# Optimization experiments

Measured on AMD Instinct MI355X. Metric: run time of the kernel, lower is better.

The kernel has to match this reference:

```python
import jax, jax.numpy as jnp
import numpy as np

# ---- static config ----
B, N, C, HF, WF = 2, 256, 256, 64, 64
PATCH = 512
ROI = 15
MARGIN = (ROI - 1) // 2
HID = 256
HEADS = 8
DEPTH = 3
FFN = 1024
NQ = 16
LN_EPS = 1e-5


def setup_inputs() -> dict:
    key = jax.random.key(0)
    ks = jax.random.split(key, 16)
    p = lambda i, shape: (0.02 * jax.random.normal(ks[i], shape, jnp.float32))
    inp = {
        "image_embeddings": jax.random.normal(ks[0], (B, C, HF, WF), jnp.float32),
        "keypoints": jax.random.uniform(ks[1], (B, N, 2), jnp.float32, 0.0, float(PATCH)),
        "keypoints_valid_mask": jax.random.randint(ks[2], (B, N), 0, 2) == 1,
        "proj_w": p(3, (HID, C)), "proj_b": jnp.zeros((HID,), jnp.float32),
        "query_embed": p(4, (NQ, HID)),
        "self_qkv_w": p(5, (DEPTH, 3 * HID, HID)), "self_qkv_b": jnp.zeros((DEPTH, 3 * HID), jnp.float32),
        "self_out_w": p(6, (DEPTH, HID, HID)), "self_out_b": jnp.zeros((DEPTH, HID), jnp.float32),
        "cross_qkv_w": p(7, (DEPTH, 3 * HID, HID)), "cross_qkv_b": jnp.zeros((DEPTH, 3 * HID), jnp.float32),
        "cross_out_w": p(8, (DEPTH, HID, HID)), "cross_out_b": jnp.zeros((DEPTH, HID), jnp.float32),
        "ffn1_w": p(9, (DEPTH, FFN, HID)), "ffn1_b": jnp.zeros((DEPTH, FFN), jnp.float32),
        "ffn2_w": p(10, (DEPTH, HID, FFN)), "ffn2_b": jnp.zeros((DEPTH, HID), jnp.float32),
        "ln1_w": jnp.ones((DEPTH, HID), jnp.float32), "ln1_b": jnp.zeros((DEPTH, HID), jnp.float32),
        "ln2_w": jnp.ones((DEPTH, HID), jnp.float32), "ln2_b": jnp.zeros((DEPTH, HID), jnp.float32),
        "ln3_w": jnp.ones((DEPTH, HID), jnp.float32), "ln3_b": jnp.zeros((DEPTH, HID), jnp.float32),
        "out_w": p(11, (4, HID)), "out_b": jnp.zeros((4,), jnp.float32),
    }
    return inp


def _layer_norm(x, w, b):
    mu = x.mean(-1, keepdims=True)
    var = ((x - mu) ** 2).mean(-1, keepdims=True)
    return (x - mu) * jax.lax.rsqrt(var + LN_EPS) * w + b


def _mha(q_in, kv_in, Wqkv, bqkv, Wo, bo, pad=None):
    # PyTorch nn.MultiheadAttention math (batch_first). pad: [B, S_kv] True=masked.
    Dh = HID // HEADS
    Wq, Wk, Wv = jnp.split(Wqkv, 3, axis=0)
    bq, bk, bv = jnp.split(bqkv, 3, axis=0)
    Bsz = q_in.shape[0]
    q = (q_in @ Wq.T + bq).reshape(Bsz, -1, HEADS, Dh)
    k = (kv_in @ Wk.T + bk).reshape(Bsz, -1, HEADS, Dh)
    v = (kv_in @ Wv.T + bv).reshape(Bsz, -1, HEADS, Dh)
    s = jnp.einsum('bqhd,bkhd->bhqk', q, k) * (Dh ** -0.5)
    if pad is not None:
        s = jnp.where(pad[:, None, None, :], -jnp.inf, s)
    a = jax.nn.softmax(s, axis=-1)
    o = jnp.einsum('bhqk,bkhd->bqhd', a, v).reshape(Bsz, -1, HID)
    return o @ Wo.T + bo


def _roi_sample(img, keypoints):
    # _get_valid_grid + F.grid_sample(bilinear, align_corners=False, zeros padding)
    rc = jnp.round(keypoints)                               # [B,N,2] (r,c), round-half-even like Python round
    off = jnp.arange(-MARGIN, MARGIN + 1, dtype=img.dtype)  # [ROI]
    gy = rc[:, :, 0][..., None, None] + off[:, None]        # [B,N,ROI,ROI] rows
    gx = rc[:, :, 1][..., None, None] + off[None, :]        # [B,N,ROI,ROI] cols
    gxn = gx / (PATCH - 1) * 2.0 - 1.0
    gyn = gy / (PATCH - 1) * 2.0 - 1.0
    invalid = (gxn < -1) | (gyn < -1) | (gxn > 1) | (gyn > 1)  # [B,N,ROI,ROI]
    gxn = jnp.where(invalid, 0.0, gxn)
    gyn = jnp.where(invalid, 0.0, gyn)
    # unnormalize onto the feature map (align_corners=False)
    x = ((gxn + 1.0) * WF - 1.0) * 0.5
    y = ((gyn + 1.0) * HF - 1.0) * 0.5
    x = x.reshape(B, -1)  # [B, P], P = N*ROI*ROI
    y = y.reshape(B, -1)
    x0f = jnp.floor(x); y0f = jnp.floor(y)
    wx = x - x0f; wy = y - y0f
    x0 = x0f.astype(jnp.int32); y0 = y0f.astype(jnp.int32)
    bidx = jnp.arange(B)[:, None]

    def tap(yi, xi, w):
        ok = (yi >= 0) & (yi < HF) & (xi >= 0) & (xi < WF)
        yc = jnp.clip(yi, 0, HF - 1)
        xc = jnp.clip(xi, 0, WF - 1)
        v = img[bidx, :, yc, xc]                 # [B,P,C] gather
        return v * (w * ok)[..., None]

    out = (tap(y0, x0, (1 - wy) * (1 - wx)) + tap(y0, x0 + 1, (1 - wy) * wx)
           + tap(y0 + 1, x0, wy * (1 - wx)) + tap(y0 + 1, x0 + 1, wy * wx))
    feat = out.reshape(B, N, ROI * ROI, C)
    feat = jnp.where(invalid.reshape(B, N, ROI * ROI)[..., None], 0.0, feat)
    return feat  # [B, N, HW, C]


def reference(image_embeddings, keypoints, keypoints_valid_mask, proj_w, proj_b,
              query_embed, self_qkv_w, self_qkv_b, self_out_w, self_out_b,
              cross_qkv_w, cross_qkv_b, cross_out_w, cross_out_b,
              ffn1_w, ffn1_b, ffn2_w, ffn2_b,
              ln1_w, ln1_b, ln2_w, ln2_b, ln3_w, ln3_b, out_w, out_b):
    feat = _roi_sample(image_embeddings, keypoints)                 # [B,N,HW,C]
    mem = jnp.einsum('bnpc,oc->bnpo', feat, proj_w) + proj_b        # 1x1 conv proj
    mem = mem.reshape(B * N, ROI * ROI, HID)
    pad = jnp.broadcast_to(~keypoints_valid_mask.reshape(-1, 1), (B * N, ROI * ROI))
    pad = pad.at[:, 0].set(False)                                    # token 0 always attendable
    tgt = jnp.broadcast_to(query_embed[None], (B * N, NQ, HID))
    for l in range(DEPTH):  # post-norm TransformerDecoderLayer, relu, eval (no dropout)
        sa = _mha(tgt, tgt, self_qkv_w[l], self_qkv_b[l], self_out_w[l], self_out_b[l])
        tgt = _layer_norm(tgt + sa, ln1_w[l], ln1_b[l])
        ca = _mha(tgt, mem, cross_qkv_w[l], cross_qkv_b[l], cross_out_w[l], cross_out_b[l], pad)
        tgt = _layer_norm(tgt + ca, ln2_w[l], ln2_b[l])
        ff = jax.nn.relu(tgt @ ffn1_w[l].T + ffn1_b[l]) @ ffn2_w[l].T + ffn2_b[l]
        tgt = _layer_norm(tgt + ff, ln3_w[l], ln3_b[l])
    out = tgt @ out_w.T + out_b                                      # [B*N, NQ, 4]
    return out.reshape(B, N, NQ, 4)
```

## Files before the change

### kernel.cpp

```cpp
#include <hip/hip_runtime.h>
#include <hip/hip_fp16.h>

#define LB __launch_bounds__(256)

typedef unsigned short u16;
typedef unsigned int   u32;
typedef __attribute__((ext_vector_type(8))) short bf16x8;
typedef __attribute__((ext_vector_type(4))) float f32x4;
typedef __attribute__((ext_vector_type(8))) u16  u16x8;

__device__ __forceinline__ u16 f2b(float f) {
    u32 u = __float_as_uint(f);
    u32 r = (u + 0x7fffu + ((u >> 16) & 1u)) >> 16;
    return (u16)r;
}
__device__ __forceinline__ float b2f(u16 h) {
    return __uint_as_float((u32)h << 16);
}

#define QSCALE 0.17677669529663687f


__global__ LB void k_wconv(const float* __restrict__ s0, const float* __restrict__ s1,
                           const float* __restrict__ s2, const float* __restrict__ s3,
                           const float* __restrict__ s4, const float* __restrict__ s5,
                           const float* __restrict__ s6, u16* __restrict__ dst,
                           const unsigned char* __restrict__ m, int* __restrict__ valid,
                           const float* __restrict__ pb,
                           const float* __restrict__ cqkv_b,
                           float* __restrict__ ckv)
{
    if (blockIdx.x >= 14336) {
        const int pblk = blockIdx.x - 14336;
        if (pblk == 0) {
            __shared__ int flag;
            if (threadIdx.x == 0) flag = 0;
            __syncthreads();
            int loc = 0;
            for (int off = threadIdx.x; off < 512; off += 256)
                if ((off & 3) != 0 && m[off] != 0) loc = 1;
            if (loc) atomicOr(&flag, 1);
            __syncthreads();
            const bool bytelay = (flag != 0);
            for (int s = threadIdx.x; s < 512; s += 256)
                valid[s] = bytelay ? (int)(m[s] != 0) : (int)(((const int*)m)[s] != 0);
        } else {
            const int l = pblk - 1;
            const float* Wv = s3 + (size_t)l * 196608 + 131072;
            const float* vb = cqkv_b + (size_t)l * 768 + 512;
            const int o = threadIdx.x;
            float c = 0.f;
            for (int cc = 0; cc < 256; cc += 4) {
                const float4 p4 = *(const float4*)(pb + cc);
                const float4 v4 = *(const float4*)(Wv + (size_t)o * 256 + cc);
                c += p4.x * v4.x + p4.y * v4.y + p4.z * v4.z + p4.w * v4.w;
            }
            ckv[l * 512 + o]       = cqkv_b[(size_t)l * 768 + o];
            ckv[l * 512 + 256 + o] = c + vb[o];
        }
        return;
    }
    const int e = blockIdx.x * 256 + threadIdx.x;
    if (e >= 3670016) return;
    float v;
    int i = e;
    if (i < 65536) v = s0[i];
    else if ((i -= 65536) < 589824) v = s1[i];
    else if ((i -= 589824) < 196608) v = s2[i];
    else if ((i -= 196608) < 589824) v = s3[i];
    else if ((i -= 589824) < 196608) v = s4[i];
    else if ((i -= 196608) < 786432) v = s5[i];
    else if ((i -= 786432) < 786432) v = s6[i];
    else if ((i -= 786432) < 393216) {
        const int l = i / 131072;
        const int r = (i - l * 131072) >> 8;
        const int c = i & 255;
        v = s3[(size_t)l * 196608 + (size_t)(256 + r) * 256 + c];
    } else {
        i -= 393216;
        v = s0[(i & 255) * 256 + (i >> 8)];
    }
    dst[e] = f2b(v);
}

__global__ LB void k_transpose(const float* __restrict__ img, u16* __restrict__ imgTb)
{
    __shared__ float tile[64][65];
    const int b  = blockIdx.z;
    const int c0 = blockIdx.y * 64;
    const int p0 = blockIdx.x * 64;
    const int t  = threadIdx.x;
    const int tr = t >> 6, tc = t & 63;
#pragma unroll
    for (int p = 0; p < 16; ++p) {
        const int i = p * 4 + tr;
        tile[i][tc] = img[((size_t)(b * 256 + c0 + i)) * 4096 + p0 + tc];
    }
    __syncthreads();
#pragma unroll
    for (int p = 0; p < 16; ++p) {
        const int jj = p * 4 + tr;
        imgTb[((size_t)(b * 4096 + p0 + jj)) * 256 + c0 + tc] = f2b(tile[tc][jj]);
    }
}

template<int BM>
__global__ LB void gemm_mfma(const u16* __restrict__ A, const u16* __restrict__ W,
                             const float* __restrict__ bias,
                             float* __restrict__ Cf, u16* __restrict__ Cb,
                             int M, int N, int K, int relu)
{
    constexpr int BN = 128;
    __shared__ u16 lds[2][(BM + BN) * 64];
    const int t = threadIdx.x;
    const int wid = t >> 6, lane = t & 63;
    const int bm = blockIdx.y * BM, bn = blockIdx.x * BN;
    const int KT = K >> 6;

    auto stage = [&](int buf, int kt) {
        const int k0 = kt * 64;
        const int rr = t >> 3;
        const int u  = t & 7;
#pragma unroll
        for (int q = 0; q < BM / 32; ++q) {
            const int r = q * 32 + rr;
            const u16* src = A + (size_t)(bm + r) * K + k0 + ((u ^ (r & 7)) << 3);
            __builtin_amdgcn_global_load_lds(
                (const __attribute__((address_space(1))) void*)src,
                (__attribute__((address_space(3))) void*)&lds[buf][q * 2048 + wid * 512],
                16, 0, 0);
        }
#pragma unroll
        for (int q = 0; q < 4; ++q) {
            const int r = q * 32 + rr;
            const u16* src = W + (size_t)(bn + r) * K + k0 + ((u ^ (r & 7)) << 3);
            __builtin_amdgcn_global_load_lds(
                (const __attribute__((address_space(1))) void*)src,
                (__attribute__((address_space(3))) void*)&lds[buf][BM * 64 + q * 2048 + wid * 512],
                16, 0, 0);
        }
    };

    const int wr = wid >> 1, wc = wid & 1;
    constexpr int MR = BM / 32;
    f32x4 acc[MR][4];
    const f32x4 z = {0.f, 0.f, 0.f, 0.f};
#pragma unroll
    for (int mi = 0; mi < MR; ++mi)
#pragma unroll
        for (int ni = 0; ni < 4; ++ni) acc[mi][ni] = z;

    const int r16 = lane & 15, kg = lane >> 4;

    stage(0, 0);
    int cur = 0;
    for (int kt = 0; kt < KT; ++kt) {
        asm volatile("s_waitcnt vmcnt(0)" ::: "memory");
        __syncthreads();
        if (kt + 1 < KT) stage(cur ^ 1, kt + 1);
        const u16* pA = lds[cur];
        const u16* pB = lds[cur] + BM * 64;
#pragma unroll
        for (int kk = 0; kk < 2; ++kk) {
            const int s = kk * 4 + kg;
            bf16x8 afr[MR], bfr[4];
#pragma unroll
            for (int mi = 0; mi < MR; ++mi) {
                const int r = wr * (BM / 2) + mi * 16 + r16;
                afr[mi] = *(const bf16x8*)(pA + r * 64 + ((s ^ (r & 7)) << 3));
            }
#pragma unroll
            for (int ni = 0; ni < 4; ++ni) {
                const int c = wc * 64 + ni * 16 + r16;
                bfr[ni] = *(const bf16x8*)(pB + c * 64 + ((s ^ (c & 7)) << 3));
            }
#pragma unroll
            for (int mi = 0; mi < MR; ++mi)
#pragma unroll
                for (int ni = 0; ni < 4; ++ni)
                    acc[mi][ni] = __builtin_amdgcn_mfma_f32_16x16x32_bf16(
                        afr[mi], bfr[ni], acc[mi][ni], 0, 0, 0);
        }
        cur ^= 1;
    }

#pragma unroll
    for (int mi = 0; mi < MR; ++mi) {
#pragma unroll
        for (int ni = 0; ni < 4; ++ni) {
            const int col = bn + wc * 64 + ni * 16 + r16;
            const float bs = bias ? bias[col] : 0.0f;
#pragma unroll
            for (int rg = 0; rg < 4; ++rg) {
                const int row = bm + wr * (BM / 2) + mi * 16 + kg * 4 + rg;
                float v = acc[mi][ni][rg] + bs;
                if (relu) v = fmaxf(v, 0.0f);
                if (Cf) Cf[(size_t)row * N + col] = v;
                if (Cb) Cb[(size_t)row * N + col] = f2b(v);
            }
        }
    }
}

__global__ LB void gemm_ln(const u16* __restrict__ A, const u16* __restrict__ W,
                           const float* __restrict__ bias,
                           float* __restrict__ tgt, u16* __restrict__ tgtb,
                           const float* __restrict__ lnw, const float* __restrict__ lnb,
                           int K,
                           const float* __restrict__ ow, const float* __restrict__ ob,
                           float* __restrict__ outp)
{
    __shared__ u16 lA[32 * 64];
    __shared__ u16 lB[256 * 64];
    __shared__ float psum[2][32];
    __shared__ float psq[2][32];
    __shared__ float hsum[2][32][4];
    const int t = threadIdx.x;
    const int wid = t >> 6, lane = t & 63;
    const int r16 = lane & 15, kg = lane >> 4;
    const int wr = wid >> 1, wc = wid & 1;
    const int bm = blockIdx.x * 32;
    const int KT = K >> 6;

    f32x4 acc[8];
    const f32x4 z = {0.f, 0.f, 0.f, 0.f};
#pragma unroll
    for (int ni = 0; ni < 8; ++ni) acc[ni] = z;

    for (int kt = 0; kt < KT; ++kt) {
        const int k0 = kt * 64;
        const int rr = t >> 3;
        const int u  = t & 7;
        {
            const int r = rr;
            const u16* src = A + (size_t)(bm + r) * K + k0 + ((u ^ (r & 7)) << 3);
            __builtin_amdgcn_global_load_lds(
                (const __attribute__((address_space(1))) void*)src,
                (__attribute__((address_space(3))) void*)&lA[wid * 512],
                16, 0, 0);
        }
#pragma unroll
        for (int q = 0; q < 8; ++q) {
            const int r = q * 32 + rr;
            const u16* src = W + (size_t)r * K + k0 + ((u ^ (r & 7)) << 3);
            __builtin_amdgcn_global_load_lds(
                (const __attribute__((address_space(1))) void*)src,
                (__attribute__((address_space(3))) void*)&lB[q * 2048 + wid * 512],
                16, 0, 0);
        }
        asm volatile("s_waitcnt vmcnt(0)" ::: "memory");
        __syncthreads();
#pragma unroll
        for (int kk = 0; kk < 2; ++kk) {
            const int s = kk * 4 + kg;
            const int ra = wr * 16 + r16;
            const bf16x8 afr = *(const bf16x8*)(lA + ra * 64 + ((s ^ (ra & 7)) << 3));
#pragma unroll
            for (int ni = 0; ni < 8; ++ni) {
                const int c = wc * 128 + ni * 16 + r16;
                const bf16x8 bfr = *(const bf16x8*)(lB + c * 64 + ((s ^ (c & 7)) << 3));
                acc[ni] = __builtin_amdgcn_mfma_f32_16x16x32_bf16(afr, bfr, acc[ni], 0, 0, 0);
            }
        }
        __syncthreads();
    }

    float xv[4][8];
    float bcol[8], wcol[8], bncol[8];
#pragma unroll
    for (int ni = 0; ni < 8; ++ni) {
        const int c = wc * 128 + ni * 16 + r16;
        bcol[ni]  = bias[c];
        wcol[ni]  = lnw[c];
        bncol[ni] = lnb[c];
    }
#pragma unroll
    for (int rg = 0; rg < 4; ++rg) {
        const int row = bm + wr * 16 + kg * 4 + rg;
#pragma unroll
        for (int ni = 0; ni < 8; ++ni) {
            const int c = wc * 128 + ni * 16 + r16;
            xv[rg][ni] = tgt[(size_t)row * 256 + c] + acc[ni][rg] + bcol[ni];
        }
    }
#pragma unroll
    for (int rg = 0; rg < 4; ++rg) {
        float s = 0.f;
#pragma unroll
        for (int ni = 0; ni < 8; ++ni) s += xv[rg][ni];
#pragma unroll
        for (int m = 1; m < 16; m <<= 1) s += __shfl_xor(s, m);
        if (r16 == 0) psum[wc][wr * 16 + kg * 4 + rg] = s;
    }
    __syncthreads();
    float mu[4];
#pragma unroll
    for (int rg = 0; rg < 4; ++rg) {
        const int rl = wr * 16 + kg * 4 + rg;
        mu[rg] = (psum[0][rl] + psum[1][rl]) * (1.0f / 256.0f);
    }
#pragma unroll
    for (int rg = 0; rg < 4; ++rg) {
        float q = 0.f;
#pragma unroll
        for (int ni = 0; ni < 8; ++ni) {
            const float d = xv[rg][ni] - mu[rg];
            q += d * d;
        }
#pragma unroll
        for (int m = 1; m < 16; m <<= 1) q += __shfl_xor(q, m);
        if (r16 == 0) psq[wc][wr * 16 + kg * 4 + rg] = q;
    }
    __syncthreads();
    float onorm[4][8];
#pragma unroll
    for (int rg = 0; rg < 4; ++rg) {
        const int rl = wr * 16 + kg * 4 + rg;
        const int row = bm + rl;
        const float var = (psq[0][rl] + psq[1][rl]) * (1.0f / 256.0f);
        const float inv = 1.0f / sqrtf(var + 1e-5f);
#pragma unroll
        for (int ni = 0; ni < 8; ++ni) {
            const int c = wc * 128 + ni * 16 + r16;
            const float o = (xv[rg][ni] - mu[rg]) * inv * wcol[ni] + bncol[ni];
            onorm[rg][ni] = o;
            tgt[(size_t)row * 256 + c]  = o;
            tgtb[(size_t)row * 256 + c] = f2b(o);
        }
    }

    if (outp) {
#pragma unroll
        for (int j = 0; j < 4; ++j) {
            float wj[8];
#pragma unroll
            for (int ni = 0; ni < 8; ++ni)
                wj[ni] = ow[j * 256 + wc * 128 + ni * 16 + r16];
#pragma unroll
            for (int rg = 0; rg < 4; ++rg) {
                float p = 0.f;
#pragma unroll
                for (int ni = 0; ni < 8; ++ni) p += onorm[rg][ni] * wj[ni];
#pragma unroll
                for (int m = 1; m < 16; m <<= 1) p += __shfl_xor(p, m);
                if (r16 == 0) hsum[wc][wr * 16 + kg * 4 + rg][j] = p;
            }
        }
        __syncthreads();
        if (t < 128) {
            const int row = t >> 2, j = t & 3;
            outp[(size_t)(bm + row) * 4 + j] =
                hsum[0][row][j] + hsum[1][row][j] + ob[j];
        }
    }
}

__global__ LB void k_init_tgt(float* __restrict__ tgt, u16* __restrict__ tgtb,
                              const float* __restrict__ qe)
{
    const int e = blockIdx.x * 256 + threadIdx.x;
    const int c = e & 255;
    const int row = e >> 8;
    const int i = row & 15;
    const float v = qe[(i << 8) | c];
    tgt[e] = v;
    tgtb[e] = f2b(v);
}

__global__ LB void k_self_attn(const u16* __restrict__ QKV, u16* __restrict__ O)
{
    __shared__ __align__(16) u16 arena[4][1536];
    const int t = threadIdx.x;
    const int lane = t & 63, wid = t >> 6;
    const int r16 = lane & 15, kg = lane >> 4;
    const int blk = blockIdx.x;
    const int s = blk >> 1;
    const int h = (blk & 1) * 4 + wid;

    u16* p_lds = &arena[wid][0];
    u16* vT    = &arena[wid][512];

    const bf16x8 qfr = *(const bf16x8*)(QKV + (size_t)(s * 16 + r16) * 768 + h * 32 + kg * 8);
    const bf16x8 kfr = *(const bf16x8*)(QKV + (size_t)(s * 16 + r16) * 768 + 256 + h * 32 + kg * 8);
    f32x4 sv = {0.f, 0.f, 0.f, 0.f};
    sv = __builtin_amdgcn_mfma_f32_16x16x32_bf16(qfr, kfr, sv, 0, 0, 0);

    float ev[4], rowsum[4];
#pragma unroll
    for (int rg = 0; rg < 4; ++rg) ev[rg] = sv[rg] * QSCALE;
#pragma unroll
    for (int rg = 0; rg < 4; ++rg) {
        float mx = ev[rg];
#pragma unroll
        for (int m = 1; m < 16; m <<= 1) mx = fmaxf(mx, __shfl_xor(mx, m));
        ev[rg] = __expf(ev[rg] - mx);
        float ps = ev[rg];
#pragma unroll
        for (int m = 1; m < 16; m <<= 1) ps += __shfl_xor(ps, m);
        rowsum[rg] = ps;
    }

#pragma unroll
    for (int rg = 0; rg < 4; ++rg)
        p_lds[(kg * 4 + rg) * 32 + r16] = f2b(ev[rg]);
    {
        const int zq = lane & 15, zc = 16 + (lane >> 4) * 4;
#pragma unroll
        for (int j = 0; j < 4; ++j) p_lds[zq * 32 + zc + j] = 0;
    }
    {
        const int key = lane >> 2, ch8 = (lane & 3) * 8;
        const u16x8 v = *(const u16x8*)(QKV + (size_t)(s * 16 + key) * 768 + 512 + h * 32 + ch8);
#pragma unroll
        for (int j = 0; j < 8; ++j)
            vT[(ch8 + j) * 32 + key] = ((const u16*)&v)[j];
        const int zc0 = lane >> 1, zk0 = 16 + (lane & 1) * 8;
#pragma unroll
        for (int j = 0; j < 8; ++j) vT[zc0 * 32 + zk0 + j] = 0;
    }

#pragma unroll
    for (int ct = 0; ct < 2; ++ct) {
        const bf16x8 pa = *(const bf16x8*)(p_lds + r16 * 32 + kg * 8);
        const bf16x8 vb = *(const bf16x8*)(vT + (ct * 16 + r16) * 32 + kg * 8);
        f32x4 ao = {0.f, 0.f, 0.f, 0.f};
        ao = __builtin_amdgcn_mfma_f32_16x16x32_bf16(pa, vb, ao, 0, 0, 0);
#pragma unroll
        for (int rg = 0; rg < 4; ++rg) {
            const int q = kg * 4 + rg;
            O[(size_t)(s * 16 + q) * 256 + h * 32 + ct * 16 + r16] = f2b(ao[rg] / rowsum[rg]);
        }
    }
}

__global__ LB void k_cross_attn(const u16* __restrict__ tgtb,
                                const u16* __restrict__ wQ,
                                const u16* __restrict__ KV, int kvs,
                                const float* __restrict__ ckv,
                                const int* __restrict__ valid,
                                const float* __restrict__ kps,
                                u16* __restrict__ O)
{
    __shared__ __align__(16) char arena[64832];
    u16* Wm  = (u16*)arena;
    u16* WmT = (u16*)(arena + 14400);

    const int t = threadIdx.x;
    const int lane = t & 63, wid = t >> 6;
    const int r16 = lane & 15, kg = lane >> 4;
    const int blk = blockIdx.x;
    const int s = blk >> 1;
    const int h = (blk & 1) * 4 + wid;
    const int b = s >> 8, n = s & 255;

    u16* buf = (u16*)(arena + 22848 + wid * 10496);
    u16* p_b = (u16*)(arena + 22848 + wid * 10496 + 2048);
    u16* QP  = p_b;

    for (int e = t; e < 16208; e += 256) ((u32*)arena)[e] = 0;
    __syncthreads();

    const float kpy = kps[(b * 256 + n) * 2 + 0];
    const float kpx = kps[(b * 256 + n) * 2 + 1];
    const float gx0 = rintf(kpx) - 7.0f;
    const float gy0 = rintf(kpy) - 7.0f;
    const float gxn0 = gx0 / 511.0f * 2.0f - 1.0f;
    const float gyn0 = gy0 / 511.0f * 2.0f - 1.0f;
    const float xb = ((gxn0 + 1.f) * 64.f - 1.f) * 0.5f;
    const float yb = ((gyn0 + 1.f) * 64.f - 1.f) * 0.5f;
    const int x0b = (int)floorf(xb);
    const int y0b = (int)floorf(yb);

    if (t < 225) {
        const int iy = t / 15, ix = t - iy * 15;
        const float gy = rintf(kpy) + (float)(iy - 7);
        const float gx = rintf(kpx) + (float)(ix - 7);
        const float gxn = gx / 511.0f * 2.0f - 1.0f;
        const float gyn = gy / 511.0f * 2.0f - 1.0f;
        const bool inval = (gxn < -1.f) || (gyn < -1.f) || (gxn > 1.f) || (gyn > 1.f);
        const float x = ((gxn + 1.f) * 64.f - 1.f) * 0.5f;
        const float y = ((gyn + 1.f) * 64.f - 1.f) * 0.5f;
        const float x0f = floorf(x), y0f = floorf(y);
        const float wx = x - x0f, wy = y - y0f;
        const int x0 = (int)x0f, y0 = (int)y0f;
#pragma unroll
        for (int tt = 0; tt < 4; ++tt) {
            const int dy = tt >> 1, dx = tt & 1;
            const int yi = y0 + dy, xi = x0 + dx;
            const bool ok = (yi >= 0) && (yi < 64) && (xi >= 0) && (xi < 64) && !inval;
            const float w = (dy ? wy : 1.f - wy) * (dx ? wx : 1.f - wx);
            if (ok) {
                const int cell = (yi - y0b) * 4 + (xi - x0b);
                const u16 wb = f2b(w);
                Wm[t * 32 + ((((cell >> 3) ^ (t & 3)) << 3) | (cell & 7))] = wb;
                WmT[cell * 264 + t] = wb;
            }
        }
    }
#pragma unroll
    for (int ct = 0; ct < 2; ++ct) {
        f32x4 aq = {0.f, 0.f, 0.f, 0.f};
#pragma unroll
        for (int ks = 0; ks < 8; ++ks) {
            const bf16x8 ta = *(const bf16x8*)(tgtb + (size_t)(s * 16 + r16) * 256 + ks * 32 + kg * 8);
            const bf16x8 wb = *(const bf16x8*)(wQ + (size_t)(h * 32 + ct * 16 + r16) * 256 + ks * 32 + kg * 8);
            aq = __builtin_amdgcn_mfma_f32_16x16x32_bf16(ta, wb, aq, 0, 0, 0);
        }
        const float bq = ckv[h * 32 + ct * 16 + r16];
#pragma unroll
        for (int rg = 0; rg < 4; ++rg)
            QP[(kg * 4 + rg) * 40 + ct * 16 + r16] = f2b(aq[rg] + bq);
    }
    const int cell = lane >> 2, ch8 = (lane & 3) * 8;
    const int cy = cell >> 2, cx = cell & 3;
    const int py = min(max(y0b + cy, 0), 63);
    const int px = min(max(x0b + cx, 0), 63);
    const size_t texidx = (size_t)(b * 4096 + py * 64 + px) * kvs + h * 32 + ch8;
    *(u16x8*)(buf + cell * 32 + ch8) = *(const u16x8*)(KV + texidx);
    const bool vld = valid[s] != 0;
    __syncthreads();

    {
        const bf16x8 qfr = *(const bf16x8*)(QP + r16 * 40 + kg * 8);
        const bf16x8 tfr = *(const bf16x8*)(buf + r16 * 32 + kg * 8);
        f32x4 aq = {0.f, 0.f, 0.f, 0.f};
        aq = __builtin_amdgcn_mfma_f32_16x16x32_bf16(qfr, tfr, aq, 0, 0, 0);
#pragma unroll
        for (int rg = 0; rg < 4; ++rg)
            QP[(kg * 4 + rg) * 40 + r16] = f2b(aq[rg]);
    }

    float ev[4][15];
    {
        const bf16x8 afr = *(const bf16x8*)(QP + r16 * 40 + kg * 8);
#pragma unroll
        for (int tile = 0; tile < 15; ++tile) {
            const int p = tile * 16 + r16;
            const int rc = p < 225 ? p : 224;
            const bf16x8 bfr = *(const bf16x8*)(Wm + rc * 32 + ((kg ^ (rc & 3)) << 3));
            f32x4 acc = {0.f, 0.f, 0.f, 0.f};
            acc = __builtin_amdgcn_mfma_f32_16x16x32_bf16(afr, bfr, acc, 0, 0, 0);
#pragma unroll
            for (int rg = 0; rg < 4; ++rg) {
                float sv = acc[rg] * QSCALE;
                if (p > 224) sv = -1e30f;
                if (!vld && p > 0) sv = -1e30f;
                ev[rg][tile] = sv;
            }
        }
    }
    float rowsumv[4];
#pragma unroll
    for (int rg = 0; rg < 4; ++rg) {
        float mx = -1e30f;
#pragma unroll
        for (int k = 0; k < 15; ++k) mx = fmaxf(mx, ev[rg][k]);
#pragma unroll
        for (int m = 1; m < 16; m <<= 1) mx = fmaxf(mx, __shfl_xor(mx, m));
        float ps = 0.f;
#pragma unroll
        for (int k = 0; k < 15; ++k) {
            ev[rg][k] = __expf(ev[rg][k] - mx);
            ps += ev[rg][k];
        }
#pragma unroll
        for (int m = 1; m < 16; m <<= 1) ps += __shfl_xor(ps, m);
        rowsumv[rg] = ps;
    }

#pragma unroll
    for (int rg = 0; rg < 4; ++rg)
#pragma unroll
        for (int k = 0; k < 15; ++k) {
            const int p = k * 16 + r16;
            if (p < 225) p_b[(kg * 4 + rg) * 264 + p] = f2b(ev[rg][k]);
        }
    for (int e = lane; e < 496; e += 64) {
        const int row = e / 31;
        p_b[row * 264 + 225 + (e - row * 31)] = 0;
    }

    {
        const u16x8 v = *(const u16x8*)(KV + texidx + 256);
#pragma unroll
        for (int j = 0; j < 8; ++j)
            buf[(ch8 + j) * 32 + cell] = ((const u16*)&v)[j];
        const int zr = lane & 15, zc0 = 16 + (lane >> 4) * 4;
#pragma unroll
        for (int j = 0; j < 4; ++j) buf[zr * 32 + zc0 + j] = 0;
    }

    f32x4 pw = {0.f, 0.f, 0.f, 0.f};
#pragma unroll
    for (int ks = 0; ks < 8; ++ks) {
        const bf16x8 pa = *(const bf16x8*)(p_b + r16 * 264 + ks * 32 + kg * 8);
        const bf16x8 wb = *(const bf16x8*)(WmT + r16 * 264 + ks * 32 + kg * 8);
        pw = __builtin_amdgcn_mfma_f32_16x16x32_bf16(pa, wb, pw, 0, 0, 0);
    }

#pragma unroll
    for (int rg = 0; rg < 4; ++rg)
        QP[(kg * 4 + rg) * 40 + r16] = f2b(pw[rg]);
    {
        const int zq = lane & 15, zc0 = 16 + (lane >> 4) * 4;
#pragma unroll
        for (int j = 0; j < 4; ++j) QP[zq * 40 + zc0 + j] = 0;
    }

#pragma unroll
    for (int ct = 0; ct < 2; ++ct) {
        const bf16x8 pa = *(const bf16x8*)(QP + r16 * 40 + kg * 8);
        const bf16x8 vb = *(const bf16x8*)(buf + (ct * 16 + r16) * 32 + kg * 8);
        f32x4 ao = {0.f, 0.f, 0.f, 0.f};
        ao = __builtin_amdgcn_mfma_f32_16x16x32_bf16(pa, vb, ao, 0, 0, 0);
#pragma unroll
        for (int rg = 0; rg < 4; ++rg) {
            const int q = kg * 4 + rg;
            const int ch = h * 32 + ct * 16 + r16;
            const float val = ao[rg] / rowsumv[rg] + ckv[256 + ch];
            O[(size_t)(s * 16 + q) * 256 + ch] = f2b(val);
        }
    }
}

extern "C" void kernel_launch(void* const* d_in, const int* in_sizes, int n_in,
                              void* d_out, int out_size, void* d_ws, size_t ws_size,
                              hipStream_t stream)
{
    const float* img          = (const float*)d_in[0];
    const float* kps          = (const float*)d_in[1];
    const unsigned char* vmsk = (const unsigned char*)d_in[2];
    const float* proj_w       = (const float*)d_in[3];
    const float* proj_b       = (const float*)d_in[4];
    const float* query_embed  = (const float*)d_in[5];
    const float* self_qkv_w   = (const float*)d_in[6];
    const float* self_qkv_b   = (const float*)d_in[7];
    const float* self_out_w   = (const float*)d_in[8];
    const float* self_out_b   = (const float*)d_in[9];
    const float* cross_qkv_w  = (const float*)d_in[10];
    const float* cross_qkv_b  = (const float*)d_in[11];
    const float* cross_out_w  = (const float*)d_in[12];
    const float* cross_out_b  = (const float*)d_in[13];
    const float* ffn1_w       = (const float*)d_in[14];
    const float* ffn1_b       = (const float*)d_in[15];
    const float* ffn2_w       = (const float*)d_in[16];
    const float* ffn2_b       = (const float*)d_in[17];
    const float* ln1_w        = (const float*)d_in[18];
    const float* ln1_b        = (const float*)d_in[19];
    const float* ln2_w        = (const float*)d_in[20];
    const float* ln2_b        = (const float*)d_in[21];
    const float* ln3_w        = (const float*)d_in[22];
    const float* ln3_b        = (const float*)d_in[23];
    const float* out_w        = (const float*)d_in[24];
    const float* out_b        = (const float*)d_in[25];
    float* out = (float*)d_out;

    char* W8 = (char*)d_ws;
    size_t off = 0;
    auto alloc = [&](size_t bytes) { void* p = W8 + off; off += (bytes + 255) & ~(size_t)255; return p; };
    float* tgt   = (float*)alloc(2097152 * 4);
    u16* Sb16    = (u16*)alloc(6291456 * 2);
    float* ckv   = (float*)alloc(3 * 512 * 4);
    u16* imgTb   = (u16*)alloc(2097152 * 2);
    u16* KVb3    = (u16*)alloc(12582912 * 2);
    u16* tgtb    = (u16*)alloc(2097152 * 2);
    u16* Abuf    = (u16*)alloc(2097152 * 2);
    u16* Hbuf    = (u16*)alloc(8388608 * 2);
    u16* wAll    = (u16*)alloc(3670016 * 2);
    u16* WcombB  = (u16*)alloc(393216 * 2);
    int* valid   = (int*)alloc(512 * 4);

    u16* wProj  = wAll;
    u16* wSQKV  = wProj + 65536;
    u16* wSOut  = wSQKV + 589824;
    u16* wCQKV  = wSOut + 196608;
    u16* wCOut  = wCQKV + 589824;
    u16* wF1    = wCOut + 196608;
    u16* wF2    = wF1 + 786432;
    u16* wCKV3  = wF2 + 786432;
    u16* wProjT = wCKV3 + 393216;

    k_wconv<<<14340, 256, 0, stream>>>(proj_w, self_qkv_w, self_out_w, cross_qkv_w,
                                       cross_out_w, ffn1_w, ffn2_w, wAll,
                                       vmsk, valid, proj_b, cross_qkv_b, ckv);
    k_transpose<<<dim3(64, 4, 2), 256, 0, stream>>>(img, imgTb);
    gemm_mfma<64><<<dim3(2, 24), 256, 0, stream>>>(wCKV3, wProjT, nullptr,
                                                   nullptr, WcombB, 1536, 256, 256, 0);
    gemm_mfma<128><<<dim3(12, 64), 256, 0, stream>>>(imgTb, WcombB, nullptr,
                                                     nullptr, KVb3, 8192, 1536, 256, 0);
    k_init_tgt<<<8192, 256, 0, stream>>>(tgt, tgtb, query_embed);

    for (int l = 0; l < 3; ++l) {
        const int last = (l == 2);
        gemm_mfma<64><<<dim3(6, 128), 256, 0, stream>>>(tgtb, wSQKV + (size_t)l * 196608,
            self_qkv_b + (size_t)l * 768, nullptr, Sb16, 8192, 768, 256, 0);
        k_self_attn<<<1024, 256, 0, stream>>>(Sb16, Abuf);
        gemm_ln<<<256, 256, 0, stream>>>(Abuf, wSOut + (size_t)l * 65536,
            self_out_b + (size_t)l * 256, tgt, tgtb,
            ln1_w + (size_t)l * 256, ln1_b + (size_t)l * 256, 256,
            nullptr, nullptr, nullptr);

        k_cross_attn<<<1024, 256, 0, stream>>>(tgtb, wCQKV + (size_t)l * 196608,
                                               KVb3 + (size_t)l * 512, 1536,
                                               ckv + (size_t)l * 512, valid, kps, Abuf);
        gemm_ln<<<256, 256, 0, stream>>>(Abuf, wCOut + (size_t)l * 65536,
            cross_out_b + (size_t)l * 256, tgt, tgtb,
            ln2_w + (size_t)l * 256, ln2_b + (size_t)l * 256, 256,
            nullptr, nullptr, nullptr);

        gemm_mfma<64><<<dim3(8, 128), 256, 0, stream>>>(tgtb, wF1 + (size_t)l * 262144,
            ffn1_b + (size_t)l * 1024, nullptr, Hbuf, 8192, 1024, 256, 1);
        gemm_ln<<<256, 256, 0, stream>>>(Hbuf, wF2 + (size_t)l * 262144,
            ffn2_b + (size_t)l * 256, tgt, tgtb,
            ln3_w + (size_t)l * 256, ln3_b + (size_t)l * 256, 1024,
            last ? out_w : nullptr, last ? out_b : nullptr, last ? out : nullptr);
    }
}
```

Measured before the change: 371.0 us.

## Fuse self-attention QKV projection into the self-attention kernel

The separate QKV GEMM and its bf16 staging buffer are removed. Each self-attention wavefront now computes its own head's Q, K and V slices with MFMA directly from tgtb and the weights, keeping them in LDS. This saves one launch per layer and a round trip of the QKV activations through global memory. In exchange each block reloads weight tiles per head without cross-block reuse, and the kernel uses more LDS. Separately, the KV precompute GEMM tile size changes from 128 to 64 with double the grid.

```diff
diff --git a/kernel.cpp b/kernel.cpp
--- a/kernel.cpp
+++ b/kernel.cpp
@@ -367,9 +367,12 @@
     tgtb[e] = f2b(v);
 }
 
-__global__ LB void k_self_attn(const u16* __restrict__ QKV, u16* __restrict__ O)
+__global__ LB void k_self_attn(const u16* __restrict__ tgtb,
+                               const u16* __restrict__ wQKV,
+                               const float* __restrict__ bqkv,
+                               u16* __restrict__ O)
 {
-    __shared__ __align__(16) u16 arena[4][1536];
+    __shared__ __align__(16) u16 arena[4][2560];
     const int t = threadIdx.x;
     const int lane = t & 63, wid = t >> 6;
     const int r16 = lane & 15, kg = lane >> 4;
@@ -377,11 +380,50 @@
     const int s = blk >> 1;
     const int h = (blk & 1) * 4 + wid;
 
-    u16* p_lds = &arena[wid][0];
-    u16* vT    = &arena[wid][512];
-
-    const bf16x8 qfr = *(const bf16x8*)(QKV + (size_t)(s * 16 + r16) * 768 + h * 32 + kg * 8);
-    const bf16x8 kfr = *(const bf16x8*)(QKV + (size_t)(s * 16 + r16) * 768 + 256 + h * 32 + kg * 8);
+    u16* q_lds = &arena[wid][0];
+    u16* k_lds = &arena[wid][512];
+    u16* vT    = &arena[wid][1024];
+    u16* p_lds = &arena[wid][2048];
+
+    bf16x8 ta[8];
+#pragma unroll
+    for (int ks = 0; ks < 8; ++ks)
+        ta[ks] = *(const bf16x8*)(tgtb + (size_t)(s * 16 + r16) * 256 + ks * 32 + kg * 8);
+
+#pragma unroll
+    for (int oi = 0; oi < 3; ++oi) {
+#pragma unroll
+        for (int ct = 0; ct < 2; ++ct) {
+            f32x4 acc = {0.f, 0.f, 0.f, 0.f};
+#pragma unroll
+            for (int ks = 0; ks < 8; ++ks) {
+                const bf16x8 wb = *(const bf16x8*)(wQKV +
+                    (size_t)(oi * 256 + h * 32 + ct * 16 + r16) * 256 + ks * 32 + kg * 8);
+                acc = __builtin_amdgcn_mfma_f32_16x16x32_bf16(ta[ks], wb, acc, 0, 0, 0);
+            }
+            const float bb = bqkv[oi * 256 + h * 32 + ct * 16 + r16];
+#pragma unroll
+            for (int rg = 0; rg < 4; ++rg) {
+                const int row = kg * 4 + rg;
+                const int ch  = ct * 16 + r16;
+                const u16 val = f2b(acc[rg] + bb);
+                if (oi == 0)      q_lds[row * 32 + ch] = val;
+                else if (oi == 1) k_lds[row * 32 + ch] = val;
+                else              vT[ch * 32 + row]    = val;
+            }
+        }
+    }
+    {
+        const int zc0 = lane >> 1, zk0 = 16 + (lane & 1) * 8;
+#pragma unroll
+        for (int j = 0; j < 8; ++j) vT[zc0 * 32 + zk0 + j] = 0;
+        const int zq = lane & 15, zc = 16 + (lane >> 4) * 4;
+#pragma unroll
+        for (int j = 0; j < 4; ++j) p_lds[zq * 32 + zc + j] = 0;
+    }
+
+    const bf16x8 qfr = *(const bf16x8*)(q_lds + r16 * 32 + kg * 8);
+    const bf16x8 kfr = *(const bf16x8*)(k_lds + r16 * 32 + kg * 8);
     f32x4 sv = {0.f, 0.f, 0.f, 0.f};
     sv = __builtin_amdgcn_mfma_f32_16x16x32_bf16(qfr, kfr, sv, 0, 0, 0);
 
@@ -403,21 +445,6 @@
 #pragma unroll
     for (int rg = 0; rg < 4; ++rg)
         p_lds[(kg * 4 + rg) * 32 + r16] = f2b(ev[rg]);
-    {
-        const int zq = lane & 15, zc = 16 + (lane >> 4) * 4;
-#pragma unroll
-        for (int j = 0; j < 4; ++j) p_lds[zq * 32 + zc + j] = 0;
-    }
-    {
-        const int key = lane >> 2, ch8 = (lane & 3) * 8;
-        const u16x8 v = *(const u16x8*)(QKV + (size_t)(s * 16 + key) * 768 + 512 + h * 32 + ch8);
-#pragma unroll
-        for (int j = 0; j < 8; ++j)
-            vT[(ch8 + j) * 32 + key] = ((const u16*)&v)[j];
-        const int zc0 = lane >> 1, zk0 = 16 + (lane & 1) * 8;
-#pragma unroll
-        for (int j = 0; j < 8; ++j) vT[zc0 * 32 + zk0 + j] = 0;
-    }
 
 #pragma unroll
     for (int ct = 0; ct < 2; ++ct) {
@@ -659,7 +686,6 @@
     size_t off = 0;
     auto alloc = [&](size_t bytes) { void* p = W8 + off; off += (bytes + 255) & ~(size_t)255; return p; };
     float* tgt   = (float*)alloc(2097152 * 4);
-    u16* Sb16    = (u16*)alloc(6291456 * 2);
     float* ckv   = (float*)alloc(3 * 512 * 4);
     u16* imgTb   = (u16*)alloc(2097152 * 2);
     u16* KVb3    = (u16*)alloc(12582912 * 2);
@@ -686,15 +712,14 @@
     k_transpose<<<dim3(64, 4, 2), 256, 0, stream>>>(img, imgTb);
     gemm_mfma<64><<<dim3(2, 24), 256, 0, stream>>>(wCKV3, wProjT, nullptr,
                                                    nullptr, WcombB, 1536, 256, 256, 0);
-    gemm_mfma<128><<<dim3(12, 64), 256, 0, stream>>>(imgTb, WcombB, nullptr,
+    gemm_mfma<64><<<dim3(12, 128), 256, 0, stream>>>(imgTb, WcombB, nullptr,
                                                      nullptr, KVb3, 8192, 1536, 256, 0);
     k_init_tgt<<<8192, 256, 0, stream>>>(tgt, tgtb, query_embed);
 
     for (int l = 0; l < 3; ++l) {
         const int last = (l == 2);
-        gemm_mfma<64><<<dim3(6, 128), 256, 0, stream>>>(tgtb, wSQKV + (size_t)l * 196608,
-            self_qkv_b + (size_t)l * 768, nullptr, Sb16, 8192, 768, 256, 0);
-        k_self_attn<<<1024, 256, 0, stream>>>(Sb16, Abuf);
+        k_self_attn<<<1024, 256, 0, stream>>>(tgtb, wSQKV + (size_t)l * 196608,
+                                              self_qkv_b + (size_t)l * 768, Abuf);
         gemm_ln<<<256, 256, 0, stream>>>(Abuf, wSOut + (size_t)l * 65536,
             self_out_b + (size_t)l * 256, tgt, tgtb,
             ln1_w + (size_t)l * 256, ln1_b + (size_t)l * 256, 256,
```

After: 406.6 us. +9.6%, slower.
